# Performance work log

Hardware: AMD Instinct MI355X
Metric: run time of the kernel (lower is better)

The kernel has to match this reference:

```python
import jax, jax.numpy as jnp
import numpy as np
from jax import lax

OBS, ACT, H, VOX = 2264, 32, 4096, 216  # voxel tail is 6*6*6


def _conv3d(v, w, b):
    # v: [1,1,6,6,6], w: [1,1,3,3,3] (OIDHW), SAME padding, stride 1
    y = lax.conv_general_dilated(v, w, window_strides=(1, 1, 1), padding='SAME',
                                 dimension_numbers=('NCDHW', 'OIDHW', 'NCDHW'))
    return jax.nn.relu(y + b.reshape(1, -1, 1, 1, 1))


def setup_inputs() -> dict:
    key = jax.random.key(0)
    ks = jax.random.split(key, 24)
    s = 0.05
    inp = {'x': jax.random.normal(ks[0], (1, OBS), dtype=jnp.float32)}
    # six Conv3d(1,1,3) kernels + biases
    for i in range(6):
        inp[f'cw{i}'] = jax.random.normal(ks[1 + i], (1, 1, 3, 3, 3), dtype=jnp.float32) * s
        inp[f'cb{i}'] = jax.random.normal(ks[7 + i], (1,), dtype=jnp.float32) * s
    # MLP: Linear(OBS->H), Linear(H->H), Linear(H->ACT); torch layout W:[out,in]
    inp['W0'] = jax.random.normal(ks[13], (H, OBS), dtype=jnp.float32) * 0.02
    inp['b0'] = jnp.zeros((H,), jnp.float32)
    inp['W1'] = jax.random.normal(ks[14], (H, H), dtype=jnp.float32) * 0.02
    inp['b1'] = jnp.zeros((H,), jnp.float32)
    inp['W2'] = jax.random.normal(ks[15], (ACT, H), dtype=jnp.float32) * 0.02
    inp['b2'] = jnp.zeros((ACT,), jnp.float32)
    # default transformations (in_shift=0, in_scale=1, out_shift=0, out_scale=1)
    inp['in_shift'] = jnp.zeros((OBS,), jnp.float32)
    inp['in_scale'] = jnp.ones((OBS,), jnp.float32)
    inp['out_shift'] = jnp.zeros((ACT,), jnp.float32)
    inp['out_scale'] = jnp.ones((ACT,), jnp.float32)
    return inp


def reference(x, cw0, cw1, cw2, cw3, cw4, cw5, cb0, cb1, cb2, cb3, cb4, cb5,
              W0, b0, W1, b1, W2, b2, in_shift, in_scale, out_shift, out_scale):
    v = x[:, -VOX:].reshape(1, 1, 6, 6, 6)
    for w, b in ((cw0, cb0), (cw1, cb1), (cw2, cb2), (cw3, cb3), (cw4, cb4), (cw5, cb5)):
        v = _conv3d(v, w, b)
    out = jnp.concatenate([x[:, :-VOX], v.reshape(1, VOX)], axis=1)
    out = (out - in_shift) / (in_scale + 1e-8)
    out = jnp.tanh(out @ W0.T + b0)
    out = jnp.tanh(out @ W1.T + b1)
    out = out @ W2.T + b2
    return out * out_scale + out_shift
```

## Files before the change

### kernel.cpp

```cpp
#include <hip/hip_runtime.h>
#include <math.h>

#define OBS 2264
#define ACT 32
#define HID 4096
#define VOX 216
#define PRE (OBS - VOX)
#define N4_OBS (OBS / 4)
#define N4_HID (HID / 4)
#define ROWS 4

__global__ __launch_bounds__(256) void fused0_kernel(
    const float* __restrict__ x,
    const float* __restrict__ cw0, const float* __restrict__ cb0,
    const float* __restrict__ cw1, const float* __restrict__ cb1,
    const float* __restrict__ cw2, const float* __restrict__ cb2,
    const float* __restrict__ cw3, const float* __restrict__ cb3,
    const float* __restrict__ cw4, const float* __restrict__ cb4,
    const float* __restrict__ cw5, const float* __restrict__ cb5,
    const float* __restrict__ in_shift, const float* __restrict__ in_scale,
    const float* __restrict__ W0, const float* __restrict__ b0,
    float* __restrict__ h0)
{
    __shared__ float skw[6][27];
    __shared__ float skb[6];
    __shared__ float vbA[VOX], vbB[VOX];
    __shared__ __align__(16) float su[OBS];
    __shared__ float part[ROWS][4];

    const int tid = threadIdx.x;

    if (tid < 27)        skw[0][tid]       = cw0[tid];
    else if (tid < 54)   skw[1][tid - 27]  = cw1[tid - 27];
    else if (tid < 81)   skw[2][tid - 54]  = cw2[tid - 54];
    else if (tid < 108)  skw[3][tid - 81]  = cw3[tid - 81];
    else if (tid < 135)  skw[4][tid - 108] = cw4[tid - 108];
    else if (tid < 162)  skw[5][tid - 135] = cw5[tid - 135];
    else if (tid == 162) skb[0] = cb0[0];
    else if (tid == 163) skb[1] = cb1[0];
    else if (tid == 164) skb[2] = cb2[0];
    else if (tid == 165) skb[3] = cb3[0];
    else if (tid == 166) skb[4] = cb4[0];
    else if (tid == 167) skb[5] = cb5[0];
    if (tid < VOX) vbA[tid] = x[PRE + tid];
    __syncthreads();

    const int d = tid / 36;
    const int h = (tid / 6) % 6;
    const int w = tid % 6;

#define CONV_LAYER(L, SRC, DST)                                              \
    if (tid < VOX) {                                                         \
        float acc = skb[L];                                                  \
        _Pragma("unroll") for (int kd = 0; kd < 3; ++kd) {                   \
            const int dd = d + kd - 1;                                       \
            if (dd >= 0 && dd <= 5) {                                        \
                _Pragma("unroll") for (int kh = 0; kh < 3; ++kh) {           \
                    const int hh = h + kh - 1;                               \
                    if (hh >= 0 && hh <= 5) {                                \
                        _Pragma("unroll") for (int kw2 = 0; kw2 < 3; ++kw2) {\
                            const int ww = w + kw2 - 1;                      \
                            if (ww >= 0 && ww <= 5)                          \
                                acc += skw[L][kd * 9 + kh * 3 + kw2]         \
                                     * SRC[dd * 36 + hh * 6 + ww];           \
                        }                                                    \
                    }                                                        \
                }                                                            \
            }                                                                \
        }                                                                    \
        DST[tid] = fmaxf(acc, 0.f);                                          \
    }                                                                        \
    __syncthreads();

    CONV_LAYER(0, vbA, vbB)
    CONV_LAYER(1, vbB, vbA)
    CONV_LAYER(2, vbA, vbB)
    CONV_LAYER(3, vbB, vbA)
    CONV_LAYER(4, vbA, vbB)
    CONV_LAYER(5, vbB, vbA)
#undef CONV_LAYER

    for (int i = tid; i < OBS; i += 256) {
        const float val = (i < PRE) ? x[i] : vbA[i - PRE];
        su[i] = (val - in_shift[i]) / (in_scale[i] + 1e-8f);
    }
    __syncthreads();

    const int row0 = blockIdx.x * ROWS;
    const float4* __restrict__ u4 = reinterpret_cast<const float4*>(su);
    const float4* __restrict__ W4 = reinterpret_cast<const float4*>(W0);
    const size_t rstride4 = OBS / 4;

    float accs[ROWS] = {0.f, 0.f, 0.f, 0.f};
    for (int j = tid; j < N4_OBS; j += 256) {
        const float4 uv = u4[j];
        #pragma unroll
        for (int r = 0; r < ROWS; ++r) {
            const float4 wv = W4[(size_t)(row0 + r) * rstride4 + j];
            accs[r] += wv.x * uv.x + wv.y * uv.y + wv.z * uv.z + wv.w * uv.w;
        }
    }
    #pragma unroll
    for (int r = 0; r < ROWS; ++r) {
        float a = accs[r];
        #pragma unroll
        for (int off = 32; off > 0; off >>= 1) a += __shfl_down(a, off, 64);
        if ((tid & 63) == 0) part[r][tid >> 6] = a;
    }
    __syncthreads();
    if (tid < ROWS) {
        const float s = part[tid][0] + part[tid][1] + part[tid][2] + part[tid][3]
                      + b0[row0 + tid];
        h0[row0 + tid] = tanhf(s);
    }
}

__global__ __launch_bounds__(256) void gemv1_kernel(
    const float* __restrict__ W, const float* __restrict__ b,
    const float* __restrict__ u, float* __restrict__ out)
{
    const int row0 = blockIdx.x * ROWS;
    const int tid = threadIdx.x;
    const float4* __restrict__ u4 = reinterpret_cast<const float4*>(u);
    const float4* __restrict__ W4 = reinterpret_cast<const float4*>(W);

    float accs[ROWS] = {0.f, 0.f, 0.f, 0.f};
    for (int j = tid; j < N4_HID; j += 256) {
        const float4 uv = u4[j];
        #pragma unroll
        for (int r = 0; r < ROWS; ++r) {
            const float4 wv = W4[(size_t)(row0 + r) * N4_HID + j];
            accs[r] += wv.x * uv.x + wv.y * uv.y + wv.z * uv.z + wv.w * uv.w;
        }
    }
    __shared__ float part[ROWS][4];
    #pragma unroll
    for (int r = 0; r < ROWS; ++r) {
        float a = accs[r];
        #pragma unroll
        for (int off = 32; off > 0; off >>= 1) a += __shfl_down(a, off, 64);
        if ((tid & 63) == 0) part[r][tid >> 6] = a;
    }
    __syncthreads();
    if (tid < ROWS) {
        const float s = part[tid][0] + part[tid][1] + part[tid][2] + part[tid][3]
                      + b[row0 + tid];
        out[row0 + tid] = tanhf(s);
    }
}

__global__ __launch_bounds__(1024) void gemv_out_kernel(
    const float* __restrict__ W, const float* __restrict__ b,
    const float* __restrict__ u,
    const float* __restrict__ oscale, const float* __restrict__ oshift,
    float* __restrict__ out)
{
    const int row = blockIdx.x;
    const int tid = threadIdx.x;
    const float4* __restrict__ Wr = reinterpret_cast<const float4*>(W + (size_t)row * HID);
    const float4* __restrict__ u4 = reinterpret_cast<const float4*>(u);

    const float4 wv = Wr[tid];
    const float4 uv = u4[tid];
    float a = wv.x * uv.x + wv.y * uv.y + wv.z * uv.z + wv.w * uv.w;

    #pragma unroll
    for (int off = 32; off > 0; off >>= 1) a += __shfl_down(a, off, 64);

    __shared__ float part[16];
    if ((tid & 63) == 0) part[tid >> 6] = a;
    __syncthreads();
    if (tid == 0) {
        float s = b[row];
        #pragma unroll
        for (int i = 0; i < 16; ++i) s += part[i];
        out[row] = s * oscale[row] + oshift[row];
    }
}

extern "C" void kernel_launch(void* const* d_in, const int* in_sizes, int n_in,
                              void* d_out, int out_size, void* d_ws, size_t ws_size,
                              hipStream_t stream) {
    const float* x = (const float*)d_in[0];

    const float* cw[6];
    const float* cb[6];
    if (in_sizes[2] == 1) {
        for (int i = 0; i < 6; ++i) {
            cw[i] = (const float*)d_in[1 + 2 * i];
            cb[i] = (const float*)d_in[2 + 2 * i];
        }
    } else {
        for (int i = 0; i < 6; ++i) {
            cw[i] = (const float*)d_in[1 + i];
            cb[i] = (const float*)d_in[7 + i];
        }
    }
    const float* W0       = (const float*)d_in[13];
    const float* b0       = (const float*)d_in[14];
    const float* W1       = (const float*)d_in[15];
    const float* b1       = (const float*)d_in[16];
    const float* W2       = (const float*)d_in[17];
    const float* b2       = (const float*)d_in[18];
    const float* in_shift = (const float*)d_in[19];
    const float* in_scale = (const float*)d_in[20];
    const float* oshift   = (const float*)d_in[21];
    const float* oscale   = (const float*)d_in[22];

    float* ws = (float*)d_ws;
    float* h0 = ws;
    float* h1 = ws + 4096;
    float* y  = (float*)d_out;

    fused0_kernel<<<HID / ROWS, 256, 0, stream>>>(
        x, cw[0], cb[0], cw[1], cb[1], cw[2], cb[2],
        cw[3], cb[3], cw[4], cb[4], cw[5], cb[5],
        in_shift, in_scale, W0, b0, h0);

    gemv1_kernel<<<HID / ROWS, 256, 0, stream>>>(W1, b1, h0, h1);
    gemv_out_kernel<<<ACT, 1024, 0, stream>>>(W2, b2, h1, oscale, oshift, y);
}
```

Measured before the change: 40.48 us.

## Split conv/normalize into single-block kernel and run layer-0 GEMV separately

Before, every one of 1024 blocks recomputed the six-layer 3D conv chain and the input normalization before doing its slice of the first GEMV. This moves that preprocessing into a single-block kernel that writes the normalized vector to workspace, followed by a plain GEMV with 8 rows per block. The aim is to remove redundant per-block serial conv work and its barriers. The cost is an extra kernel launch and a global round-trip for the input vector.

```diff
diff --git a/kernel.cpp b/kernel.cpp
--- a/kernel.cpp
+++ b/kernel.cpp
@@ -8,9 +8,10 @@
 #define PRE (OBS - VOX)
 #define N4_OBS (OBS / 4)
 #define N4_HID (HID / 4)
-#define ROWS 4
-
-__global__ __launch_bounds__(256) void fused0_kernel(
+#define ROWS0 8
+#define ROWS1 4
+
+__global__ __launch_bounds__(256) void conv_norm_kernel(
     const float* __restrict__ x,
     const float* __restrict__ cw0, const float* __restrict__ cb0,
     const float* __restrict__ cw1, const float* __restrict__ cb1,
@@ -19,29 +20,34 @@
     const float* __restrict__ cw4, const float* __restrict__ cb4,
     const float* __restrict__ cw5, const float* __restrict__ cb5,
     const float* __restrict__ in_shift, const float* __restrict__ in_scale,
-    const float* __restrict__ W0, const float* __restrict__ b0,
-    float* __restrict__ h0)
+    float* __restrict__ u)
 {
     __shared__ float skw[6][27];
     __shared__ float skb[6];
     __shared__ float vbA[VOX], vbB[VOX];
-    __shared__ __align__(16) float su[OBS];
-    __shared__ float part[ROWS][4];
-
-    const int tid = threadIdx.x;
-
-    if (tid < 27)        skw[0][tid]       = cw0[tid];
-    else if (tid < 54)   skw[1][tid - 27]  = cw1[tid - 27];
-    else if (tid < 81)   skw[2][tid - 54]  = cw2[tid - 54];
-    else if (tid < 108)  skw[3][tid - 81]  = cw3[tid - 81];
-    else if (tid < 135)  skw[4][tid - 108] = cw4[tid - 108];
-    else if (tid < 162)  skw[5][tid - 135] = cw5[tid - 135];
-    else if (tid == 162) skb[0] = cb0[0];
-    else if (tid == 163) skb[1] = cb1[0];
-    else if (tid == 164) skb[2] = cb2[0];
-    else if (tid == 165) skb[3] = cb3[0];
-    else if (tid == 166) skb[4] = cb4[0];
-    else if (tid == 167) skb[5] = cb5[0];
+
+    const int tid = threadIdx.x;
+
+    if (tid < 162) {
+        const float* srcw = tid < 27  ? cw0
+                          : tid < 54  ? cw1
+                          : tid < 81  ? cw2
+                          : tid < 108 ? cw3
+                          : tid < 135 ? cw4 : cw5;
+        const int base = tid < 27  ? 0
+                       : tid < 54  ? 27
+                       : tid < 81  ? 54
+                       : tid < 108 ? 81
+                       : tid < 135 ? 108 : 135;
+        reinterpret_cast<float*>(skw)[tid] = srcw[tid - base];
+    } else if (tid >= 192 && tid < 198) {
+        const float* srcb = tid == 192 ? cb0
+                          : tid == 193 ? cb1
+                          : tid == 194 ? cb2
+                          : tid == 195 ? cb3
+                          : tid == 196 ? cb4 : cb5;
+        skb[tid - 192] = srcb[0];
+    }
     if (tid < VOX) vbA[tid] = x[PRE + tid];
     __syncthreads();
 
@@ -82,36 +88,45 @@
 
     for (int i = tid; i < OBS; i += 256) {
         const float val = (i < PRE) ? x[i] : vbA[i - PRE];
-        su[i] = (val - in_shift[i]) / (in_scale[i] + 1e-8f);
-    }
-    __syncthreads();
-
-    const int row0 = blockIdx.x * ROWS;
-    const float4* __restrict__ u4 = reinterpret_cast<const float4*>(su);
-    const float4* __restrict__ W4 = reinterpret_cast<const float4*>(W0);
-    const size_t rstride4 = OBS / 4;
-
-    float accs[ROWS] = {0.f, 0.f, 0.f, 0.f};
+        u[i] = (val - in_shift[i]) / (in_scale[i] + 1e-8f);
+    }
+}
+
+__global__ __launch_bounds__(256) void gemv0_kernel(
+    const float* __restrict__ W, const float* __restrict__ b,
+    const float* __restrict__ u, float* __restrict__ out)
+{
+    const int row0 = blockIdx.x * ROWS0;
+    const int tid = threadIdx.x;
+    const float4* __restrict__ u4 = reinterpret_cast<const float4*>(u);
+    const float4* __restrict__ W4 = reinterpret_cast<const float4*>(W);
+
+    float accs[ROWS0];
+    #pragma unroll
+    for (int r = 0; r < ROWS0; ++r) accs[r] = 0.f;
+
     for (int j = tid; j < N4_OBS; j += 256) {
         const float4 uv = u4[j];
         #pragma unroll
-        for (int r = 0; r < ROWS; ++r) {
-            const float4 wv = W4[(size_t)(row0 + r) * rstride4 + j];
+        for (int r = 0; r < ROWS0; ++r) {
+            const float4 wv = W4[(size_t)(row0 + r) * N4_OBS + j];
             accs[r] += wv.x * uv.x + wv.y * uv.y + wv.z * uv.z + wv.w * uv.w;
         }
     }
-    #pragma unroll
-    for (int r = 0; r < ROWS; ++r) {
+
+    __shared__ float part[ROWS0][4];
+    #pragma unroll
+    for (int r = 0; r < ROWS0; ++r) {
         float a = accs[r];
         #pragma unroll
         for (int off = 32; off > 0; off >>= 1) a += __shfl_down(a, off, 64);
         if ((tid & 63) == 0) part[r][tid >> 6] = a;
     }
     __syncthreads();
-    if (tid < ROWS) {
+    if (tid < ROWS0) {
         const float s = part[tid][0] + part[tid][1] + part[tid][2] + part[tid][3]
-                      + b0[row0 + tid];
-        h0[row0 + tid] = tanhf(s);
+                      + b[row0 + tid];
+        out[row0 + tid] = tanhf(s);
     }
 }
 
@@ -119,30 +134,30 @@
     const float* __restrict__ W, const float* __restrict__ b,
     const float* __restrict__ u, float* __restrict__ out)
 {
-    const int row0 = blockIdx.x * ROWS;
+    const int row0 = blockIdx.x * ROWS1;
     const int tid = threadIdx.x;
     const float4* __restrict__ u4 = reinterpret_cast<const float4*>(u);
     const float4* __restrict__ W4 = reinterpret_cast<const float4*>(W);
 
-    float accs[ROWS] = {0.f, 0.f, 0.f, 0.f};
+    float accs[ROWS1] = {0.f, 0.f, 0.f, 0.f};
     for (int j = tid; j < N4_HID; j += 256) {
         const float4 uv = u4[j];
         #pragma unroll
-        for (int r = 0; r < ROWS; ++r) {
+        for (int r = 0; r < ROWS1; ++r) {
             const float4 wv = W4[(size_t)(row0 + r) * N4_HID + j];
             accs[r] += wv.x * uv.x + wv.y * uv.y + wv.z * uv.z + wv.w * uv.w;
         }
     }
-    __shared__ float part[ROWS][4];
-    #pragma unroll
-    for (int r = 0; r < ROWS; ++r) {
+    __shared__ float part[ROWS1][4];
+    #pragma unroll
+    for (int r = 0; r < ROWS1; ++r) {
         float a = accs[r];
         #pragma unroll
         for (int off = 32; off > 0; off >>= 1) a += __shfl_down(a, off, 64);
         if ((tid & 63) == 0) part[r][tid >> 6] = a;
     }
     __syncthreads();
-    if (tid < ROWS) {
+    if (tid < ROWS1) {
         const float s = part[tid][0] + part[tid][1] + part[tid][2] + part[tid][3]
                       + b[row0 + tid];
         out[row0 + tid] = tanhf(s);
@@ -208,15 +223,17 @@
     const float* oscale   = (const float*)d_in[22];
 
     float* ws = (float*)d_ws;
-    float* h0 = ws;
-    float* h1 = ws + 4096;
+    float* u  = ws;
+    float* h0 = ws + 2304;
+    float* h1 = ws + 6400;
     float* y  = (float*)d_out;
 
-    fused0_kernel<<<HID / ROWS, 256, 0, stream>>>(
+    conv_norm_kernel<<<1, 256, 0, stream>>>(
         x, cw[0], cb[0], cw[1], cb[1], cw[2], cb[2],
         cw[3], cb[3], cw[4], cb[4], cw[5], cb[5],
-        in_shift, in_scale, W0, b0, h0);
-
-    gemv1_kernel<<<HID / ROWS, 256, 0, stream>>>(W1, b1, h0, h1);
+        in_shift, in_scale, u);
+
+    gemv0_kernel<<<HID / ROWS0, 256, 0, stream>>>(W0, b0, u, h0);
+    gemv1_kernel<<<HID / ROWS1, 256, 0, stream>>>(W1, b1, h0, h1);
     gemv_out_kernel<<<ACT, 1024, 0, stream>>>(W2, b2, h1, oscale, oshift, y);
 }
```

Result: no change. 41.26 us (+1.9%).
